# Optimization experiments

Measured on AMD Instinct MI355X. Metric: run time of the kernel, lower is better.

The kernel has to match this reference:

```python
import jax, jax.numpy as jnp
import numpy as np

BETA = 0.95
THETA = 1.0  # snn.Leaky default threshold
SLOPE = 25.0  # fast_sigmoid surrogate slope

@jax.custom_vjp
def spike_fn(v):
    # Heaviside forward, fast-sigmoid surrogate backward (snntorch surrogate.fast_sigmoid)
    return (v > 0).astype(v.dtype)

def _spike_fwd(v):
    return spike_fn(v), v

def _spike_bwd(v, g):
    return (g / (SLOPE * jnp.abs(v) + 1.0) ** 2,)

spike_fn.defvjp(_spike_fwd, _spike_bwd)


def setup_inputs() -> dict:
    key = jax.random.key(0)
    k = jax.random.split(key, 5)
    T, B, n_in, n_hid, n_out = 500, 256, 96, 64, 80  # n_out = 4 classes * 20 pop
    x = jax.random.uniform(k[0], (T, B, n_in), dtype=jnp.float32)
    s1 = 1.0 / np.sqrt(n_in)
    s2 = 1.0 / np.sqrt(n_hid)
    W1 = jax.random.uniform(k[1], (n_in, n_hid), jnp.float32, -s1, s1)
    b1 = jax.random.uniform(k[2], (n_hid,), jnp.float32, -s1, s1)
    W2 = jax.random.uniform(k[3], (n_hid, n_out), jnp.float32, -s2, s2)
    b2 = jax.random.uniform(k[4], (n_out,), jnp.float32, -s2, s2)
    return {"x": x, "W1": W1, "b1": b1, "W2": W2, "b2": b2}


def reference(x, W1, b1, W2, b2):
    # Dropout is in eval mode (identity). snntorch Leaky with reset_mechanism='subtract':
    #   reset_t = spk_{t-1};  mem_t = beta*mem_{t-1} + cur_t - reset_t*theta;  spk_t = H(mem_t - theta)
    B = x.shape[1]
    n_hid = W1.shape[1]
    n_out = W2.shape[1]
    z_h = jnp.zeros((B, n_hid), x.dtype)
    z_o = jnp.zeros((B, n_out), x.dtype)

    def step(carry, xt):
        mem1, spk1, mem2, spk2 = carry
        cur1 = xt @ W1 + b1
        mem1 = BETA * mem1 + cur1 - spk1 * THETA
        spk1 = spike_fn(mem1 - THETA)
        cur2 = spk1 @ W2 + b2
        mem2 = BETA * mem2 + cur2 - spk2 * THETA
        spk2 = spike_fn(mem2 - THETA)
        return (mem1, spk1, mem2, spk2), (spk2, mem2)

    _, (spk_out, mem_out) = jax.lax.scan(step, (z_h, z_h, z_o, z_o), x)
    return spk_out, mem_out
```

## Files before the change

### kernel.cpp

```cpp
#include <hip/hip_runtime.h>


#define T_STEPS 500
#define BATCH   256
#define N_IN    96
#define N_HID   64
#define N_OUT   80
#define CH      50

__global__ __launch_bounds__(256) void k1_cur1(
    const float* __restrict__ x,
    const float* __restrict__ W1,
    const float* __restrict__ b1,
    float* __restrict__ cur1)
{
    const int tp   = blockIdx.x >> 2;
    const int b0   = (blockIdx.x & 3) << 6;
    const int t0   = tp * 2;
    const int lane = threadIdx.x & 63;
    const int w    = threadIdx.x >> 6;
    const int o0   = w << 4;

    __shared__ float sm[18944];

    {
        const float4* __restrict__ s0 =
            reinterpret_cast<const float4*>(x + ((size_t)t0 * BATCH + b0) * N_IN);
        const float4* __restrict__ s1 =
            reinterpret_cast<const float4*>(x + ((size_t)(t0 + 1) * BATCH + b0) * N_IN);
        #pragma unroll
        for (int ii = 0; ii < 6; ++ii) {
            const int i = ii * 256 + threadIdx.x;
            const float4 v0 = s0[i], v1 = s1[i];
            const int row = i / 24, g = i % 24;
            *reinterpret_cast<float4*>(&sm[row * 100 + g * 4]) = v0;
            *reinterpret_cast<float4*>(&sm[6400 + row * 100 + g * 4]) = v1;
        }
        const float4* __restrict__ srcw = reinterpret_cast<const float4*>(W1);
        #pragma unroll
        for (int ii = 0; ii < 6; ++ii) {
            const int i = ii * 256 + threadIdx.x;
            *reinterpret_cast<float4*>(&sm[12800 + i * 4]) = srcw[i];
        }
    }
    __syncthreads();

    float acc0[16], acc1[16];
    #pragma unroll
    for (int o = 0; o < 16; ++o) { acc0[o] = 0.0f; acc1[o] = 0.0f; }

    const int xb = lane * 100;
    #pragma unroll 2
    for (int kg = 0; kg < 24; ++kg) {
        const float4 xv0 = *reinterpret_cast<const float4*>(&sm[xb + kg * 4]);
        const float4 xv1 = *reinterpret_cast<const float4*>(&sm[6400 + xb + kg * 4]);
        const float xq0[4] = {xv0.x, xv0.y, xv0.z, xv0.w};
        const float xq1[4] = {xv1.x, xv1.y, xv1.z, xv1.w};
        #pragma unroll
        for (int jj = 0; jj < 4; ++jj) {
            const int k = kg * 4 + jj;
            const float4* __restrict__ wr =
                reinterpret_cast<const float4*>(&sm[12800 + k * 64 + o0]);
            const float4 w0 = wr[0], w1 = wr[1], w2 = wr[2], w3 = wr[3];
            const float xs0 = xq0[jj], xs1 = xq1[jj];
            acc0[0]  = __fmaf_rn(xs0, w0.x, acc0[0]);
            acc0[1]  = __fmaf_rn(xs0, w0.y, acc0[1]);
            acc0[2]  = __fmaf_rn(xs0, w0.z, acc0[2]);
            acc0[3]  = __fmaf_rn(xs0, w0.w, acc0[3]);
            acc0[4]  = __fmaf_rn(xs0, w1.x, acc0[4]);
            acc0[5]  = __fmaf_rn(xs0, w1.y, acc0[5]);
            acc0[6]  = __fmaf_rn(xs0, w1.z, acc0[6]);
            acc0[7]  = __fmaf_rn(xs0, w1.w, acc0[7]);
            acc0[8]  = __fmaf_rn(xs0, w2.x, acc0[8]);
            acc0[9]  = __fmaf_rn(xs0, w2.y, acc0[9]);
            acc0[10] = __fmaf_rn(xs0, w2.z, acc0[10]);
            acc0[11] = __fmaf_rn(xs0, w2.w, acc0[11]);
            acc0[12] = __fmaf_rn(xs0, w3.x, acc0[12]);
            acc0[13] = __fmaf_rn(xs0, w3.y, acc0[13]);
            acc0[14] = __fmaf_rn(xs0, w3.z, acc0[14]);
            acc0[15] = __fmaf_rn(xs0, w3.w, acc0[15]);
            acc1[0]  = __fmaf_rn(xs1, w0.x, acc1[0]);
            acc1[1]  = __fmaf_rn(xs1, w0.y, acc1[1]);
            acc1[2]  = __fmaf_rn(xs1, w0.z, acc1[2]);
            acc1[3]  = __fmaf_rn(xs1, w0.w, acc1[3]);
            acc1[4]  = __fmaf_rn(xs1, w1.x, acc1[4]);
            acc1[5]  = __fmaf_rn(xs1, w1.y, acc1[5]);
            acc1[6]  = __fmaf_rn(xs1, w1.z, acc1[6]);
            acc1[7]  = __fmaf_rn(xs1, w1.w, acc1[7]);
            acc1[8]  = __fmaf_rn(xs1, w2.x, acc1[8]);
            acc1[9]  = __fmaf_rn(xs1, w2.y, acc1[9]);
            acc1[10] = __fmaf_rn(xs1, w2.z, acc1[10]);
            acc1[11] = __fmaf_rn(xs1, w2.w, acc1[11]);
            acc1[12] = __fmaf_rn(xs1, w3.x, acc1[12]);
            acc1[13] = __fmaf_rn(xs1, w3.y, acc1[13]);
            acc1[14] = __fmaf_rn(xs1, w3.z, acc1[14]);
            acc1[15] = __fmaf_rn(xs1, w3.w, acc1[15]);
        }
    }

    __syncthreads();
    #pragma unroll
    for (int o4 = 0; o4 < 4; ++o4) {
        float4 v0, v1;
        v0.x = __fadd_rn(acc0[o4 * 4 + 0], b1[o0 + o4 * 4 + 0]);
        v0.y = __fadd_rn(acc0[o4 * 4 + 1], b1[o0 + o4 * 4 + 1]);
        v0.z = __fadd_rn(acc0[o4 * 4 + 2], b1[o0 + o4 * 4 + 2]);
        v0.w = __fadd_rn(acc0[o4 * 4 + 3], b1[o0 + o4 * 4 + 3]);
        v1.x = __fadd_rn(acc1[o4 * 4 + 0], b1[o0 + o4 * 4 + 0]);
        v1.y = __fadd_rn(acc1[o4 * 4 + 1], b1[o0 + o4 * 4 + 1]);
        v1.z = __fadd_rn(acc1[o4 * 4 + 2], b1[o0 + o4 * 4 + 2]);
        v1.w = __fadd_rn(acc1[o4 * 4 + 3], b1[o0 + o4 * 4 + 3]);
        *reinterpret_cast<float4*>(&sm[lane * 68 + o0 + o4 * 4]) = v0;
        *reinterpret_cast<float4*>(&sm[6400 + lane * 68 + o0 + o4 * 4]) = v1;
    }
    __syncthreads();
    {
        float4* __restrict__ d0 =
            reinterpret_cast<float4*>(cur1 + ((size_t)t0 * BATCH + b0) * N_HID);
        float4* __restrict__ d1 =
            reinterpret_cast<float4*>(cur1 + ((size_t)(t0 + 1) * BATCH + b0) * N_HID);
        #pragma unroll
        for (int ii = 0; ii < 4; ++ii) {
            const int i = ii * 256 + threadIdx.x;
            const int row = i / 16, g = i % 16;
            d0[i] = *reinterpret_cast<const float4*>(&sm[row * 68 + g * 4]);
            d1[i] = *reinterpret_cast<const float4*>(&sm[6400 + row * 68 + g * 4]);
        }
    }
}

__global__ __launch_bounds__(64) void k2_rec1(float* cs)
{
    const int b = blockIdx.x;
    const int h = threadIdx.x;
    const size_t str  = (size_t)BATCH * N_HID;
    const size_t base = (size_t)b * N_HID + h;

    float A[CH], Bv[CH];
    #pragma unroll
    for (int i = 0; i < CH; ++i) A[i] = cs[(size_t)i * str + base];

    float mem = 0.f, s = 0.f;
    for (int cp = 0; cp < 5; ++cp) {
        const int c0 = 2 * cp;
        #pragma unroll
        for (int i = 0; i < CH; ++i)
            Bv[i] = cs[(size_t)((c0 + 1) * CH + i) * str + base];
        #pragma unroll
        for (int i = 0; i < CH; ++i) {
            const float m = __fsub_rn(__fadd_rn(__fmul_rn(0.95f, mem), A[i]), s);
            mem = m; s = (m > 1.0f) ? 1.0f : 0.0f;
            cs[(size_t)(c0 * CH + i) * str + base] = s;
        }
        if (cp < 4) {
            #pragma unroll
            for (int i = 0; i < CH; ++i)
                A[i] = cs[(size_t)((c0 + 2) * CH + i) * str + base];
        }
        #pragma unroll
        for (int i = 0; i < CH; ++i) {
            const float m = __fsub_rn(__fadd_rn(__fmul_rn(0.95f, mem), Bv[i]), s);
            mem = m; s = (m > 1.0f) ? 1.0f : 0.0f;
            cs[(size_t)((c0 + 1) * CH + i) * str + base] = s;
        }
    }
}

__global__ __launch_bounds__(256) void k3_cur2(
    const float* __restrict__ spk,
    const float* __restrict__ W2,
    const float* __restrict__ b2,
    float* __restrict__ cur2)
{
    const int tp   = blockIdx.x >> 2;
    const int b0   = (blockIdx.x & 3) << 6;
    const int t0   = tp * 2;
    const int lane = threadIdx.x & 63;
    const int w    = threadIdx.x >> 6;
    const int o0   = w * 20;

    __shared__ float sm[13824];

    {
        const float4* __restrict__ s0 =
            reinterpret_cast<const float4*>(spk + ((size_t)t0 * BATCH + b0) * N_HID);
        const float4* __restrict__ s1 =
            reinterpret_cast<const float4*>(spk + ((size_t)(t0 + 1) * BATCH + b0) * N_HID);
        #pragma unroll
        for (int ii = 0; ii < 4; ++ii) {
            const int i = ii * 256 + threadIdx.x;
            const float4 v0 = s0[i], v1 = s1[i];
            const int row = i / 16, g = i % 16;
            *reinterpret_cast<float4*>(&sm[row * 68 + g * 4]) = v0;
            *reinterpret_cast<float4*>(&sm[4352 + row * 68 + g * 4]) = v1;
        }
        const float4* __restrict__ srcw = reinterpret_cast<const float4*>(W2);
        for (int i = threadIdx.x; i < 1280; i += 256)
            *reinterpret_cast<float4*>(&sm[8704 + i * 4]) = srcw[i];
    }
    __syncthreads();

    float acc0[20], acc1[20];
    #pragma unroll
    for (int o = 0; o < 20; ++o) { acc0[o] = 0.0f; acc1[o] = 0.0f; }

    const int xb0 = lane * 68;
    const int xb1 = 4352 + lane * 68;
    #pragma unroll 2
    for (int kg = 0; kg < 16; ++kg) {
        const float4 xv0 = *reinterpret_cast<const float4*>(&sm[xb0 + kg * 4]);
        const float4 xv1 = *reinterpret_cast<const float4*>(&sm[xb1 + kg * 4]);
        const float xq0[4] = {xv0.x, xv0.y, xv0.z, xv0.w};
        const float xq1[4] = {xv1.x, xv1.y, xv1.z, xv1.w};
        #pragma unroll
        for (int jj = 0; jj < 4; ++jj) {
            const int k = kg * 4 + jj;
            const float4* __restrict__ wr =
                reinterpret_cast<const float4*>(&sm[8704 + k * 80 + o0]);
            const float4 w0 = wr[0], w1 = wr[1], w2 = wr[2], w3 = wr[3], w4 = wr[4];
            const float a = xq0[jj], b = xq1[jj];
            acc0[0]  = __fmaf_rn(a, w0.x, acc0[0]);
            acc0[1]  = __fmaf_rn(a, w0.y, acc0[1]);
            acc0[2]  = __fmaf_rn(a, w0.z, acc0[2]);
            acc0[3]  = __fmaf_rn(a, w0.w, acc0[3]);
            acc0[4]  = __fmaf_rn(a, w1.x, acc0[4]);
            acc0[5]  = __fmaf_rn(a, w1.y, acc0[5]);
            acc0[6]  = __fmaf_rn(a, w1.z, acc0[6]);
            acc0[7]  = __fmaf_rn(a, w1.w, acc0[7]);
            acc0[8]  = __fmaf_rn(a, w2.x, acc0[8]);
            acc0[9]  = __fmaf_rn(a, w2.y, acc0[9]);
            acc0[10] = __fmaf_rn(a, w2.z, acc0[10]);
            acc0[11] = __fmaf_rn(a, w2.w, acc0[11]);
            acc0[12] = __fmaf_rn(a, w3.x, acc0[12]);
            acc0[13] = __fmaf_rn(a, w3.y, acc0[13]);
            acc0[14] = __fmaf_rn(a, w3.z, acc0[14]);
            acc0[15] = __fmaf_rn(a, w3.w, acc0[15]);
            acc0[16] = __fmaf_rn(a, w4.x, acc0[16]);
            acc0[17] = __fmaf_rn(a, w4.y, acc0[17]);
            acc0[18] = __fmaf_rn(a, w4.z, acc0[18]);
            acc0[19] = __fmaf_rn(a, w4.w, acc0[19]);
            acc1[0]  = __fmaf_rn(b, w0.x, acc1[0]);
            acc1[1]  = __fmaf_rn(b, w0.y, acc1[1]);
            acc1[2]  = __fmaf_rn(b, w0.z, acc1[2]);
            acc1[3]  = __fmaf_rn(b, w0.w, acc1[3]);
            acc1[4]  = __fmaf_rn(b, w1.x, acc1[4]);
            acc1[5]  = __fmaf_rn(b, w1.y, acc1[5]);
            acc1[6]  = __fmaf_rn(b, w1.z, acc1[6]);
            acc1[7]  = __fmaf_rn(b, w1.w, acc1[7]);
            acc1[8]  = __fmaf_rn(b, w2.x, acc1[8]);
            acc1[9]  = __fmaf_rn(b, w2.y, acc1[9]);
            acc1[10] = __fmaf_rn(b, w2.z, acc1[10]);
            acc1[11] = __fmaf_rn(b, w2.w, acc1[11]);
            acc1[12] = __fmaf_rn(b, w3.x, acc1[12]);
            acc1[13] = __fmaf_rn(b, w3.y, acc1[13]);
            acc1[14] = __fmaf_rn(b, w3.z, acc1[14]);
            acc1[15] = __fmaf_rn(b, w3.w, acc1[15]);
            acc1[16] = __fmaf_rn(b, w4.x, acc1[16]);
            acc1[17] = __fmaf_rn(b, w4.y, acc1[17]);
            acc1[18] = __fmaf_rn(b, w4.z, acc1[18]);
            acc1[19] = __fmaf_rn(b, w4.w, acc1[19]);
        }
    }

    __syncthreads();
    #pragma unroll
    for (int o4 = 0; o4 < 5; ++o4) {
        float4 v0, v1;
        v0.x = __fadd_rn(acc0[o4 * 4 + 0], b2[o0 + o4 * 4 + 0]);
        v0.y = __fadd_rn(acc0[o4 * 4 + 1], b2[o0 + o4 * 4 + 1]);
        v0.z = __fadd_rn(acc0[o4 * 4 + 2], b2[o0 + o4 * 4 + 2]);
        v0.w = __fadd_rn(acc0[o4 * 4 + 3], b2[o0 + o4 * 4 + 3]);
        v1.x = __fadd_rn(acc1[o4 * 4 + 0], b2[o0 + o4 * 4 + 0]);
        v1.y = __fadd_rn(acc1[o4 * 4 + 1], b2[o0 + o4 * 4 + 1]);
        v1.z = __fadd_rn(acc1[o4 * 4 + 2], b2[o0 + o4 * 4 + 2]);
        v1.w = __fadd_rn(acc1[o4 * 4 + 3], b2[o0 + o4 * 4 + 3]);
        *reinterpret_cast<float4*>(&sm[lane * 84 + o0 + o4 * 4]) = v0;
        *reinterpret_cast<float4*>(&sm[5376 + lane * 84 + o0 + o4 * 4]) = v1;
    }
    __syncthreads();
    {
        float4* __restrict__ d0 =
            reinterpret_cast<float4*>(cur2 + ((size_t)t0 * BATCH + b0) * N_OUT);
        float4* __restrict__ d1 =
            reinterpret_cast<float4*>(cur2 + ((size_t)(t0 + 1) * BATCH + b0) * N_OUT);
        #pragma unroll
        for (int ii = 0; ii < 5; ++ii) {
            const int i = ii * 256 + threadIdx.x;
            const int row = i / 20, g = i % 20;
            d0[i] = *reinterpret_cast<const float4*>(&sm[row * 84 + g * 4]);
            d1[i] = *reinterpret_cast<const float4*>(&sm[5376 + row * 84 + g * 4]);
        }
    }
}

__global__ __launch_bounds__(80) void k4_rec2(float* cm, float* os)
{
    const int b = blockIdx.x;
    const int o = threadIdx.x;
    const size_t str  = (size_t)BATCH * N_OUT;
    const size_t base = (size_t)b * N_OUT + o;

    float A[CH], Bv[CH];
    #pragma unroll
    for (int i = 0; i < CH; ++i) A[i] = cm[(size_t)i * str + base];

    float mem = 0.f, s = 0.f;
    for (int cp = 0; cp < 5; ++cp) {
        const int c0 = 2 * cp;
        #pragma unroll
        for (int i = 0; i < CH; ++i)
            Bv[i] = cm[(size_t)((c0 + 1) * CH + i) * str + base];
        #pragma unroll
        for (int i = 0; i < CH; ++i) {
            const int t = c0 * CH + i;
            const float m = __fsub_rn(__fadd_rn(__fmul_rn(0.95f, mem), A[i]), s);
            mem = m; s = (m > 1.0f) ? 1.0f : 0.0f;
            os[(size_t)t * str + base] = s;
            cm[(size_t)t * str + base] = m;
        }
        if (cp < 4) {
            #pragma unroll
            for (int i = 0; i < CH; ++i)
                A[i] = cm[(size_t)((c0 + 2) * CH + i) * str + base];
        }
        #pragma unroll
        for (int i = 0; i < CH; ++i) {
            const int t = (c0 + 1) * CH + i;
            const float m = __fsub_rn(__fadd_rn(__fmul_rn(0.95f, mem), Bv[i]), s);
            mem = m; s = (m > 1.0f) ? 1.0f : 0.0f;
            os[(size_t)t * str + base] = s;
            cm[(size_t)t * str + base] = m;
        }
    }
}

extern "C" void kernel_launch(void* const* d_in, const int* in_sizes, int n_in,
                              void* d_out, int out_size, void* d_ws, size_t ws_size,
                              hipStream_t stream) {
    const float* x  = (const float*)d_in[0];
    const float* W1 = (const float*)d_in[1];
    const float* b1 = (const float*)d_in[2];
    const float* W2 = (const float*)d_in[3];
    const float* b2 = (const float*)d_in[4];
    float* outs = (float*)d_out;
    float* outm = outs + (size_t)T_STEPS * BATCH * N_OUT;

    k1_cur1<<<250 * 4, 256, 0, stream>>>(x, W1, b1, outs);
    k2_rec1<<<BATCH, 64, 0, stream>>>(outs);
    k3_cur2<<<250 * 4, 256, 0, stream>>>(outs, W2, b2, outm);
    k4_rec2<<<BATCH, 80, 0, stream>>>(outm, outs);
}
```

Baseline: 97.11 us.

## Pack layer-1 spikes into ballot bitmasks and compute four timesteps per block in cur2

The hidden-layer recurrence no longer writes float spikes back over the cur1 buffer. It uses a wavefront ballot to emit one 64-bit mask per (t,b), stored in spare output space at MASK_OFF. The cur2 GEMM reads these masks directly instead of staging float spikes through shared memory, handles four timesteps per block with half the grid, and stores results straight to global without an LDS transpose. This cuts spike traffic by about 32x, but the direct stores are less coalesced, register pressure rises with four accumulator sets, and parallelism drops.

```diff
diff --git a/kernel.cpp b/kernel.cpp
--- a/kernel.cpp
+++ b/kernel.cpp
@@ -7,6 +7,7 @@
 #define N_HID   64
 #define N_OUT   80
 #define CH      50
+#define MASK_OFF 8192000
 
 __global__ __launch_bounds__(256) void k1_cur1(
     const float* __restrict__ x,
@@ -129,7 +130,9 @@
     }
 }
 
-__global__ __launch_bounds__(64) void k2_rec1(float* cs)
+__global__ __launch_bounds__(64) void k2_rec1(
+    const float* __restrict__ cs,
+    unsigned long long* __restrict__ masks)
 {
     const int b = blockIdx.x;
     const int h = threadIdx.x;
@@ -150,7 +153,8 @@
         for (int i = 0; i < CH; ++i) {
             const float m = __fsub_rn(__fadd_rn(__fmul_rn(0.95f, mem), A[i]), s);
             mem = m; s = (m > 1.0f) ? 1.0f : 0.0f;
-            cs[(size_t)(c0 * CH + i) * str + base] = s;
+            const unsigned long long bal = __ballot(m > 1.0f);
+            if (h == 0) masks[(size_t)(c0 * CH + i) * BATCH + b] = bal;
         }
         if (cp < 4) {
             #pragma unroll
@@ -161,135 +165,106 @@
         for (int i = 0; i < CH; ++i) {
             const float m = __fsub_rn(__fadd_rn(__fmul_rn(0.95f, mem), Bv[i]), s);
             mem = m; s = (m > 1.0f) ? 1.0f : 0.0f;
-            cs[(size_t)((c0 + 1) * CH + i) * str + base] = s;
+            const unsigned long long bal = __ballot(m > 1.0f);
+            if (h == 0) masks[(size_t)((c0 + 1) * CH + i) * BATCH + b] = bal;
         }
     }
 }
 
 __global__ __launch_bounds__(256) void k3_cur2(
-    const float* __restrict__ spk,
+    const unsigned long long* __restrict__ masks,
     const float* __restrict__ W2,
     const float* __restrict__ b2,
     float* __restrict__ cur2)
 {
-    const int tp   = blockIdx.x >> 2;
+    const int tq   = blockIdx.x >> 2;
     const int b0   = (blockIdx.x & 3) << 6;
-    const int t0   = tp * 2;
+    const int t0   = tq * 4;
     const int lane = threadIdx.x & 63;
     const int w    = threadIdx.x >> 6;
     const int o0   = w * 20;
 
-    __shared__ float sm[13824];
+    __shared__ float ws[64 * 80];
 
     {
-        const float4* __restrict__ s0 =
-            reinterpret_cast<const float4*>(spk + ((size_t)t0 * BATCH + b0) * N_HID);
-        const float4* __restrict__ s1 =
-            reinterpret_cast<const float4*>(spk + ((size_t)(t0 + 1) * BATCH + b0) * N_HID);
-        #pragma unroll
-        for (int ii = 0; ii < 4; ++ii) {
+        const float4* __restrict__ srcw = reinterpret_cast<const float4*>(W2);
+        #pragma unroll
+        for (int ii = 0; ii < 5; ++ii) {
             const int i = ii * 256 + threadIdx.x;
-            const float4 v0 = s0[i], v1 = s1[i];
-            const int row = i / 16, g = i % 16;
-            *reinterpret_cast<float4*>(&sm[row * 68 + g * 4]) = v0;
-            *reinterpret_cast<float4*>(&sm[4352 + row * 68 + g * 4]) = v1;
-        }
-        const float4* __restrict__ srcw = reinterpret_cast<const float4*>(W2);
-        for (int i = threadIdx.x; i < 1280; i += 256)
-            *reinterpret_cast<float4*>(&sm[8704 + i * 4]) = srcw[i];
-    }
+            *reinterpret_cast<float4*>(&ws[i * 4]) = srcw[i];
+        }
+    }
+
+    unsigned long long mk0, mk1, mk2, mk3;
+    mk0 = masks[(size_t)(t0 + 0) * BATCH + b0 + lane];
+    mk1 = masks[(size_t)(t0 + 1) * BATCH + b0 + lane];
+    mk2 = masks[(size_t)(t0 + 2) * BATCH + b0 + lane];
+    mk3 = masks[(size_t)(t0 + 3) * BATCH + b0 + lane];
     __syncthreads();
 
-    float acc0[20], acc1[20];
-    #pragma unroll
-    for (int o = 0; o < 20; ++o) { acc0[o] = 0.0f; acc1[o] = 0.0f; }
-
-    const int xb0 = lane * 68;
-    const int xb1 = 4352 + lane * 68;
+    float acc0[20], acc1[20], acc2[20], acc3[20];
+    #pragma unroll
+    for (int o = 0; o < 20; ++o) {
+        acc0[o] = 0.0f; acc1[o] = 0.0f; acc2[o] = 0.0f; acc3[o] = 0.0f;
+    }
+
     #pragma unroll 2
     for (int kg = 0; kg < 16; ++kg) {
-        const float4 xv0 = *reinterpret_cast<const float4*>(&sm[xb0 + kg * 4]);
-        const float4 xv1 = *reinterpret_cast<const float4*>(&sm[xb1 + kg * 4]);
-        const float xq0[4] = {xv0.x, xv0.y, xv0.z, xv0.w};
-        const float xq1[4] = {xv1.x, xv1.y, xv1.z, xv1.w};
         #pragma unroll
         for (int jj = 0; jj < 4; ++jj) {
             const int k = kg * 4 + jj;
             const float4* __restrict__ wr =
-                reinterpret_cast<const float4*>(&sm[8704 + k * 80 + o0]);
+                reinterpret_cast<const float4*>(&ws[k * 80 + o0]);
             const float4 w0 = wr[0], w1 = wr[1], w2 = wr[2], w3 = wr[3], w4 = wr[4];
-            const float a = xq0[jj], b = xq1[jj];
-            acc0[0]  = __fmaf_rn(a, w0.x, acc0[0]);
-            acc0[1]  = __fmaf_rn(a, w0.y, acc0[1]);
-            acc0[2]  = __fmaf_rn(a, w0.z, acc0[2]);
-            acc0[3]  = __fmaf_rn(a, w0.w, acc0[3]);
-            acc0[4]  = __fmaf_rn(a, w1.x, acc0[4]);
-            acc0[5]  = __fmaf_rn(a, w1.y, acc0[5]);
-            acc0[6]  = __fmaf_rn(a, w1.z, acc0[6]);
-            acc0[7]  = __fmaf_rn(a, w1.w, acc0[7]);
-            acc0[8]  = __fmaf_rn(a, w2.x, acc0[8]);
-            acc0[9]  = __fmaf_rn(a, w2.y, acc0[9]);
-            acc0[10] = __fmaf_rn(a, w2.z, acc0[10]);
-            acc0[11] = __fmaf_rn(a, w2.w, acc0[11]);
-            acc0[12] = __fmaf_rn(a, w3.x, acc0[12]);
-            acc0[13] = __fmaf_rn(a, w3.y, acc0[13]);
-            acc0[14] = __fmaf_rn(a, w3.z, acc0[14]);
-            acc0[15] = __fmaf_rn(a, w3.w, acc0[15]);
-            acc0[16] = __fmaf_rn(a, w4.x, acc0[16]);
-            acc0[17] = __fmaf_rn(a, w4.y, acc0[17]);
-            acc0[18] = __fmaf_rn(a, w4.z, acc0[18]);
-            acc0[19] = __fmaf_rn(a, w4.w, acc0[19]);
-            acc1[0]  = __fmaf_rn(b, w0.x, acc1[0]);
-            acc1[1]  = __fmaf_rn(b, w0.y, acc1[1]);
-            acc1[2]  = __fmaf_rn(b, w0.z, acc1[2]);
-            acc1[3]  = __fmaf_rn(b, w0.w, acc1[3]);
-            acc1[4]  = __fmaf_rn(b, w1.x, acc1[4]);
-            acc1[5]  = __fmaf_rn(b, w1.y, acc1[5]);
-            acc1[6]  = __fmaf_rn(b, w1.z, acc1[6]);
-            acc1[7]  = __fmaf_rn(b, w1.w, acc1[7]);
-            acc1[8]  = __fmaf_rn(b, w2.x, acc1[8]);
-            acc1[9]  = __fmaf_rn(b, w2.y, acc1[9]);
-            acc1[10] = __fmaf_rn(b, w2.z, acc1[10]);
-            acc1[11] = __fmaf_rn(b, w2.w, acc1[11]);
-            acc1[12] = __fmaf_rn(b, w3.x, acc1[12]);
-            acc1[13] = __fmaf_rn(b, w3.y, acc1[13]);
-            acc1[14] = __fmaf_rn(b, w3.z, acc1[14]);
-            acc1[15] = __fmaf_rn(b, w3.w, acc1[15]);
-            acc1[16] = __fmaf_rn(b, w4.x, acc1[16]);
-            acc1[17] = __fmaf_rn(b, w4.y, acc1[17]);
-            acc1[18] = __fmaf_rn(b, w4.z, acc1[18]);
-            acc1[19] = __fmaf_rn(b, w4.w, acc1[19]);
-        }
-    }
-
-    __syncthreads();
+            const float wv[20] = {w0.x, w0.y, w0.z, w0.w,
+                                  w1.x, w1.y, w1.z, w1.w,
+                                  w2.x, w2.y, w2.z, w2.w,
+                                  w3.x, w3.y, w3.z, w3.w,
+                                  w4.x, w4.y, w4.z, w4.w};
+            const float s0 = (float)((mk0 >> k) & 1ULL);
+            const float s1 = (float)((mk1 >> k) & 1ULL);
+            const float s2 = (float)((mk2 >> k) & 1ULL);
+            const float s3 = (float)((mk3 >> k) & 1ULL);
+            #pragma unroll
+            for (int o = 0; o < 20; ++o) {
+                acc0[o] = __fmaf_rn(s0, wv[o], acc0[o]);
+                acc1[o] = __fmaf_rn(s1, wv[o], acc1[o]);
+                acc2[o] = __fmaf_rn(s2, wv[o], acc2[o]);
+                acc3[o] = __fmaf_rn(s3, wv[o], acc3[o]);
+            }
+        }
+    }
+
     #pragma unroll
     for (int o4 = 0; o4 < 5; ++o4) {
-        float4 v0, v1;
-        v0.x = __fadd_rn(acc0[o4 * 4 + 0], b2[o0 + o4 * 4 + 0]);
-        v0.y = __fadd_rn(acc0[o4 * 4 + 1], b2[o0 + o4 * 4 + 1]);
-        v0.z = __fadd_rn(acc0[o4 * 4 + 2], b2[o0 + o4 * 4 + 2]);
-        v0.w = __fadd_rn(acc0[o4 * 4 + 3], b2[o0 + o4 * 4 + 3]);
-        v1.x = __fadd_rn(acc1[o4 * 4 + 0], b2[o0 + o4 * 4 + 0]);
-        v1.y = __fadd_rn(acc1[o4 * 4 + 1], b2[o0 + o4 * 4 + 1]);
-        v1.z = __fadd_rn(acc1[o4 * 4 + 2], b2[o0 + o4 * 4 + 2]);
-        v1.w = __fadd_rn(acc1[o4 * 4 + 3], b2[o0 + o4 * 4 + 3]);
-        *reinterpret_cast<float4*>(&sm[lane * 84 + o0 + o4 * 4]) = v0;
-        *reinterpret_cast<float4*>(&sm[5376 + lane * 84 + o0 + o4 * 4]) = v1;
-    }
-    __syncthreads();
-    {
-        float4* __restrict__ d0 =
-            reinterpret_cast<float4*>(cur2 + ((size_t)t0 * BATCH + b0) * N_OUT);
-        float4* __restrict__ d1 =
-            reinterpret_cast<float4*>(cur2 + ((size_t)(t0 + 1) * BATCH + b0) * N_OUT);
-        #pragma unroll
-        for (int ii = 0; ii < 5; ++ii) {
-            const int i = ii * 256 + threadIdx.x;
-            const int row = i / 20, g = i % 20;
-            d0[i] = *reinterpret_cast<const float4*>(&sm[row * 84 + g * 4]);
-            d1[i] = *reinterpret_cast<const float4*>(&sm[5376 + row * 84 + g * 4]);
-        }
+        const float bb0 = b2[o0 + o4 * 4 + 0], bb1 = b2[o0 + o4 * 4 + 1];
+        const float bb2 = b2[o0 + o4 * 4 + 2], bb3 = b2[o0 + o4 * 4 + 3];
+        float4 v;
+        float* d;
+        v.x = __fadd_rn(acc0[o4 * 4 + 0], bb0);
+        v.y = __fadd_rn(acc0[o4 * 4 + 1], bb1);
+        v.z = __fadd_rn(acc0[o4 * 4 + 2], bb2);
+        v.w = __fadd_rn(acc0[o4 * 4 + 3], bb3);
+        d = cur2 + ((size_t)(t0 + 0) * BATCH + b0 + lane) * N_OUT + o0;
+        reinterpret_cast<float4*>(d)[o4] = v;
+        v.x = __fadd_rn(acc1[o4 * 4 + 0], bb0);
+        v.y = __fadd_rn(acc1[o4 * 4 + 1], bb1);
+        v.z = __fadd_rn(acc1[o4 * 4 + 2], bb2);
+        v.w = __fadd_rn(acc1[o4 * 4 + 3], bb3);
+        d = cur2 + ((size_t)(t0 + 1) * BATCH + b0 + lane) * N_OUT + o0;
+        reinterpret_cast<float4*>(d)[o4] = v;
+        v.x = __fadd_rn(acc2[o4 * 4 + 0], bb0);
+        v.y = __fadd_rn(acc2[o4 * 4 + 1], bb1);
+        v.z = __fadd_rn(acc2[o4 * 4 + 2], bb2);
+        v.w = __fadd_rn(acc2[o4 * 4 + 3], bb3);
+        d = cur2 + ((size_t)(t0 + 2) * BATCH + b0 + lane) * N_OUT + o0;
+        reinterpret_cast<float4*>(d)[o4] = v;
+        v.x = __fadd_rn(acc3[o4 * 4 + 0], bb0);
+        v.y = __fadd_rn(acc3[o4 * 4 + 1], bb1);
+        v.z = __fadd_rn(acc3[o4 * 4 + 2], bb2);
+        v.w = __fadd_rn(acc3[o4 * 4 + 3], bb3);
+        d = cur2 + ((size_t)(t0 + 3) * BATCH + b0 + lane) * N_OUT + o0;
+        reinterpret_cast<float4*>(d)[o4] = v;
     }
 }
 
@@ -344,9 +319,11 @@
     const float* b2 = (const float*)d_in[4];
     float* outs = (float*)d_out;
     float* outm = outs + (size_t)T_STEPS * BATCH * N_OUT;
+    unsigned long long* masks =
+        (unsigned long long*)(outs + MASK_OFF);
 
     k1_cur1<<<250 * 4, 256, 0, stream>>>(x, W1, b1, outs);
-    k2_rec1<<<BATCH, 64, 0, stream>>>(outs);
-    k3_cur2<<<250 * 4, 256, 0, stream>>>(outs, W2, b2, outm);
+    k2_rec1<<<BATCH, 64, 0, stream>>>(outs, masks);
+    k3_cur2<<<125 * 4, 256, 0, stream>>>(masks, W2, b2, outm);
     k4_rec2<<<BATCH, 80, 0, stream>>>(outm, outs);
 }
```

Measured after the change: 107.3 us. +10.5%, slower.
